# Kernel optimization log

Measured on AMD Instinct MI355X. Metric: run time of the kernel, lower is better.

## Reference

```python
import jax, jax.numpy as jnp
import numpy as np

L, D, H, N, R = 4, 256, 512, 16, 8  # layers, d_model, hidden=2*d_model, state_dim, dt_rank
OUT_LEN, IN_DIM = 96, 32
EPS = 1e-5


def _layernorm(v, g, b):
    m = jnp.mean(v, axis=-1, keepdims=True)
    var = jnp.mean((v - m) ** 2, axis=-1, keepdims=True)
    return (v - m) / jnp.sqrt(var + EPS) * g + b


def _pos_encoding(T, d):
    pos = jnp.arange(T, dtype=jnp.float32)[:, None]
    div = jnp.exp(jnp.arange(0, d, 2, dtype=jnp.float32) * (-np.log(10000.0) / d))
    pe = jnp.zeros((T, d), dtype=jnp.float32)
    pe = pe.at[:, 0::2].set(jnp.sin(pos * div))
    pe = pe.at[:, 1::2].set(jnp.cos(pos * div))
    return pe


def setup_inputs() -> dict:
    key = jax.random.key(0)
    ks = jax.random.split(key, 20)
    inp = {
        "x": jax.random.normal(ks[0], (8, 1024, IN_DIM), dtype=jnp.float32),
        "emb_w": jax.random.normal(ks[1], (D, IN_DIM), dtype=jnp.float32) * 0.1,
        "emb_b": jnp.zeros((D,), dtype=jnp.float32),
        "norm_g": jnp.ones((L, D), dtype=jnp.float32),
        "norm_b": jnp.zeros((L, D), dtype=jnp.float32),
        "in_w": jax.random.normal(ks[2], (L, H, D), dtype=jnp.float32) * (1.0 / np.sqrt(D)),
        "conv_w": jax.random.normal(ks[3], (L, H, 1, 3), dtype=jnp.float32) * 0.5,
        "A_p": jax.random.normal(ks[4], (L, H, N), dtype=jnp.float32) * 0.01,
        "D_p": jnp.ones((L, H), dtype=jnp.float32),
        "dt1_w": jax.random.normal(ks[5], (L, R, H), dtype=jnp.float32) * (1.0 / np.sqrt(H)),
        "dt1_b": jnp.zeros((L, R), dtype=jnp.float32),
        "dt2_w": jax.random.normal(ks[6], (L, H, R), dtype=jnp.float32) * (1.0 / np.sqrt(R)),
        "dt2_b": jnp.zeros((L, H), dtype=jnp.float32),
        "out_w": jax.random.normal(ks[7], (L, D, H), dtype=jnp.float32) * (1.0 / np.sqrt(H)),
        "final_g": jnp.ones((D,), dtype=jnp.float32),
        "final_b": jnp.zeros((D,), dtype=jnp.float32),
        "head1_w": jax.random.normal(ks[8], (D, D), dtype=jnp.float32) * (1.0 / np.sqrt(D)),
        "head1_b": jnp.zeros((D,), dtype=jnp.float32),
        "head2_w": jax.random.normal(ks[9], (OUT_LEN, D), dtype=jnp.float32) * (1.0 / np.sqrt(D)),
        "head2_b": jnp.zeros((OUT_LEN,), dtype=jnp.float32),
    }
    return inp


def _mamba_block(h, g, b, in_w, conv_w, A_p, D_p, dt1_w, dt1_b, dt2_w, dt2_b, out_w):
    res = h
    v = _layernorm(h, g, b)            # [B,T,D]
    v = jnp.einsum('btd,hd->bth', v, in_w)  # [B,T,H]
    # depthwise conv1d, kernel 3, padding 1, groups=H
    vc = jnp.transpose(v, (0, 2, 1))   # [B,H,T]
    vc = jax.lax.conv_general_dilated(vc, conv_w, window_strides=(1,),
                                      padding=[(1, 1)], feature_group_count=H,
                                      dimension_numbers=('NCH', 'OIH', 'NCH'))
    v = jnp.transpose(jax.nn.silu(vc), (0, 2, 1))  # [B,T,H]
    dt = jax.nn.relu(jnp.einsum('bth,rh->btr', v, dt1_w) + dt1_b)
    dt = jnp.einsum('btr,hr->bth', dt, dt2_w) + dt2_b
    dt = jax.nn.softplus(dt)           # [B,T,H]
    A = -jnp.exp(A_p)                  # [H,N]
    safe_A = jnp.where(jnp.abs(A) < 1e-5, jnp.ones_like(A), A)

    B_sz = v.shape[0]
    state0 = jnp.zeros((B_sz, H, N), dtype=v.dtype)

    def step(state, inp):
        x_t, dt_t = inp  # [B,H] each
        dA = A * dt_t[..., None]            # [B,H,N]
        discA = jnp.exp(dA)
        discB = (discA - 1.0) / safe_A * dt_t[..., None]
        state = discA * state + discB * x_t[..., None]
        y = jnp.einsum('bhn,hn->bh', state, A_p) + D_p * x_t
        return state, y

    xs = (jnp.transpose(v, (1, 0, 2)), jnp.transpose(dt, (1, 0, 2)))  # [T,B,H]
    _, ys = jax.lax.scan(step, state0, xs)
    y = jnp.transpose(ys, (1, 0, 2))   # [B,T,H]
    return res + jnp.einsum('bth,dh->btd', y, out_w)


def reference(x, emb_w, emb_b, norm_g, norm_b, in_w, conv_w, A_p, D_p,
              dt1_w, dt1_b, dt2_w, dt2_b, out_w, final_g, final_b,
              head1_w, head1_b, head2_w, head2_b):
    h = jnp.einsum('bti,di->btd', x, emb_w) + emb_b  # [B,T,D]
    h = h + _pos_encoding(h.shape[1], D)[None]
    for l in range(L):
        h = _mamba_block(h, norm_g[l], norm_b[l], in_w[l], conv_w[l], A_p[l],
                         D_p[l], dt1_w[l], dt1_b[l], dt2_w[l], dt2_b[l], out_w[l])
    h = _layernorm(h, final_g, final_b)
    h = h[:, -1, :]                    # last token [B,D]
    h = jax.nn.silu(h @ head1_w.T + head1_b)
    return h @ head2_w.T + head2_b     # [B, OUT_LEN]
```

## Files before the change

kernel.cpp:

```cpp
#include <hip/hip_runtime.h>
#include <hip/hip_bf16.h>
#include <math.h>

#define BB 8
#define TT 1024
#define DD 256
#define HH 512
#define NN 16
#define RR 8
#define OUT_LEN 96
#define IN_DIM 32
#define MM (BB*TT)

#define SC 16
#define CC (TT/SC)

typedef unsigned short u16;
typedef unsigned int u32;
typedef __attribute__((ext_vector_type(8))) short short8;
typedef __attribute__((ext_vector_type(8))) unsigned short u16x8;
typedef __attribute__((ext_vector_type(4))) float float4v;

__device__ __forceinline__ u16 f2bf(float f) {
    __hip_bfloat16 h = __float2bfloat16(f);
    return *(u16*)&h;
}
__device__ __forceinline__ float bf2f(u16 u) {
    u32 v = ((u32)u) << 16;
    return *(float*)&v;
}

#define GLD_LDS16(src, dst) __builtin_amdgcn_global_load_lds( \
    (const __attribute__((address_space(1))) void*)(src),     \
    (__attribute__((address_space(3))) void*)(dst), 16, 0, 0)

__global__ __launch_bounds__(256) void embed_ln_cvt_kernel(
    const float* __restrict__ x, const float* __restrict__ emb_w,
    const float* __restrict__ emb_b,
    const float* __restrict__ g, const float* __restrict__ b,
    float* __restrict__ h, u16* __restrict__ lnout,
    const float* __restrict__ w_in, u16* __restrict__ wbf_in,
    const float* __restrict__ w_out, u16* __restrict__ wbf_out, int nw)
{
    int bid = blockIdx.x;
    if (bid >= MM) {
        int i = (bid - MM) * 256 + threadIdx.x;
        if (i < nw) wbf_in[i] = f2bf(w_in[i]);
        else        wbf_out[i - nw] = f2bf(w_out[i - nw]);
        return;
    }

    int bt = bid;
    int d  = threadIdx.x;
    int t  = bt & (TT - 1);

    __shared__ float xs[IN_DIM];
    __shared__ float red[4], red2[4];
    if (threadIdx.x < IN_DIM) xs[threadIdx.x] = x[bt * IN_DIM + threadIdx.x];
    __syncthreads();

    const float* w = emb_w + d * IN_DIM;
    float acc = emb_b[d];
#pragma unroll
    for (int i = 0; i < IN_DIM; i++) acc = fmaf(xs[i], w[i], acc);

    int i2 = d & ~1;
    float div = __expf(-(float)i2 * 0.0359778918f);
    float arg = (float)t * div;
    float pe = (d & 1) ? __cosf(arg) : __sinf(arg);
    float val = acc + pe;
    h[bt * DD + d] = val;

    float s = val;
#pragma unroll
    for (int o = 32; o > 0; o >>= 1) s += __shfl_down(s, o);
    int lane = d & 63, wave = d >> 6;
    if (lane == 0) red[wave] = s;
    __syncthreads();
    float mean = (red[0] + red[1] + red[2] + red[3]) * (1.0f / DD);

    float c = val - mean;
    float s2 = c * c;
#pragma unroll
    for (int o = 32; o > 0; o >>= 1) s2 += __shfl_down(s2, o);
    if (lane == 0) red2[wave] = s2;
    __syncthreads();
    float var = (red2[0] + red2[1] + red2[2] + red2[3]) * (1.0f / DD);

    lnout[bt * DD + d] = f2bf(c * rsqrtf(var + 1e-5f) * g[d] + b[d]);
}

template<int BM, int BN, int OUT_BF16>
__global__ __launch_bounds__(256) void gemm_bf16(
    const u16* __restrict__ A, const u16* __restrict__ B,
    void* __restrict__ Cv, int M, int N, int K, int addC)
{
    constexpr int BK = 64;
    constexpr int MT = BM / 32;
    constexpr int NT = BN / 32;
    static_assert(BN == 64, "B staging assumes BN==64");

    __shared__ __align__(16) u16 Al[8][BM][8];
    __shared__ __align__(16) u16 Bl[8][BN][8];

    const int tid = threadIdx.x;
    const int nbx = gridDim.x;
    const int o   = blockIdx.x + nbx * blockIdx.y;
    const int r8  = o & 7, q8 = o >> 3;
    const int bxs = q8 % nbx;
    const int bys = (q8 / nbx) * 8 + r8;
    const int bm = bys * BM;
    const int bn = bxs * BN;
    const int wid = tid >> 6, lane = tid & 63;
    const int wm = wid >> 1, wn = wid & 1;
    const int lq = lane >> 4, lm = lane & 15;

    float4v acc[MT][NT];
#pragma unroll
    for (int i = 0; i < MT; i++)
#pragma unroll
        for (int j = 0; j < NT; j++) acc[i][j] = (float4v){0.f, 0.f, 0.f, 0.f};

    for (int k0 = 0; k0 < K; k0 += BK) {
#pragma unroll
        for (int it = 0; it < (8 * BM) / 256; it++) {
            int c = it * 256 + tid;
            int q = c / BM, row = c % BM;
            GLD_LDS16(A + (size_t)(bm + row) * K + k0 + q * 8, &Al[q][row][0]);
        }
#pragma unroll
        for (int it = 0; it < (8 * BN) / 256; it++) {
            int c = it * 256 + tid;
            int q = c / BN, row = c % BN;
            GLD_LDS16(B + (size_t)(bn + row) * K + k0 + q * 8, &Bl[q][row][0]);
        }
        __syncthreads();

        short8 af[2][MT], bf[2][NT];
#pragma unroll
        for (int kk = 0; kk < 2; kk++) {
#pragma unroll
            for (int mt = 0; mt < MT; mt++)
                af[kk][mt] = *(const short8*)&Al[kk * 4 + lq][wm * (BM / 2) + mt * 16 + lm][0];
#pragma unroll
            for (int nt = 0; nt < NT; nt++)
                bf[kk][nt] = *(const short8*)&Bl[kk * 4 + lq][wn * (BN / 2) + nt * 16 + lm][0];
        }

#pragma unroll
        for (int kk = 0; kk < 2; kk++)
#pragma unroll
            for (int mt = 0; mt < MT; mt++)
#pragma unroll
                for (int nt = 0; nt < NT; nt++)
                    acc[mt][nt] = __builtin_amdgcn_mfma_f32_16x16x32_bf16(
                        af[kk][mt], bf[kk][nt], acc[mt][nt], 0, 0, 0);
        __syncthreads();
    }

#pragma unroll
    for (int mt = 0; mt < MT; mt++)
#pragma unroll
        for (int nt = 0; nt < NT; nt++) {
            int row0 = bm + wm * (BM / 2) + mt * 16 + lq * 4;
            int col  = bn + wn * (BN / 2) + nt * 16 + lm;
#pragma unroll
            for (int r = 0; r < 4; r++) {
                float vv = acc[mt][nt][r];
                if (OUT_BF16) {
                    ((u16*)Cv)[(size_t)(row0 + r) * N + col] = f2bf(vv);
                } else {
                    float* cp = (float*)Cv + (size_t)(row0 + r) * N + col;
                    if (addC) vv += *cp;
                    *cp = vv;
                }
            }
        }
}

__global__ __launch_bounds__(256) void gemm2_ln(
    const u16* __restrict__ A, const u16* __restrict__ B,
    float* __restrict__ h,
    const float* __restrict__ g, const float* __restrict__ bb,
    u16* __restrict__ lnout, int doLN)
{
    constexpr int BM = 32;
    __shared__ __align__(16) u16 Al[8][BM][8];
    __shared__ __align__(16) u16 Bl[8][256][8];
    __shared__ float rs[2][BM], qs[2][BM];

    const int tid = threadIdx.x;
    const int bm = blockIdx.x * BM;
    const int wid = tid >> 6, lane = tid & 63;
    const int wm = wid >> 1, wn = wid & 1;
    const int lq = lane >> 4, lm = lane & 15;

    float4v acc[8];
#pragma unroll
    for (int j = 0; j < 8; j++) acc[j] = (float4v){0.f, 0.f, 0.f, 0.f};

    for (int k0 = 0; k0 < 512; k0 += 64) {
        {
            int q = tid >> 5, row = tid & 31;
            GLD_LDS16(A + (size_t)(bm + row) * 512 + k0 + q * 8, &Al[q][row][0]);
        }
#pragma unroll
        for (int it = 0; it < 8; it++) {
            int c = it * 256 + tid;
            int q = c >> 8, row = c & 255;
            GLD_LDS16(B + (size_t)row * 512 + k0 + q * 8, &Bl[q][row][0]);
        }
        __syncthreads();

        short8 af[2], bf[2][8];
#pragma unroll
        for (int kk = 0; kk < 2; kk++) {
            af[kk] = *(const short8*)&Al[kk * 4 + lq][wm * 16 + lm][0];
#pragma unroll
            for (int nt = 0; nt < 8; nt++)
                bf[kk][nt] = *(const short8*)&Bl[kk * 4 + lq][wn * 128 + nt * 16 + lm][0];
        }
#pragma unroll
        for (int kk = 0; kk < 2; kk++)
#pragma unroll
            for (int nt = 0; nt < 8; nt++)
                acc[nt] = __builtin_amdgcn_mfma_f32_16x16x32_bf16(
                    af[kk], bf[kk][nt], acc[nt], 0, 0, 0);
        __syncthreads();
    }

    float val[4][8];
    float s1[4] = {0.f, 0.f, 0.f, 0.f}, s2[4] = {0.f, 0.f, 0.f, 0.f};
#pragma unroll
    for (int r = 0; r < 4; r++) {
        int row = bm + wm * 16 + lq * 4 + r;
#pragma unroll
        for (int nt = 0; nt < 8; nt++) {
            int col = wn * 128 + nt * 16 + lm;
            float v = acc[nt][r] + h[(size_t)row * DD + col];
            val[r][nt] = v;
            s1[r] += v;
            s2[r] = fmaf(v, v, s2[r]);
            h[(size_t)row * DD + col] = v;
        }
    }
#pragma unroll
    for (int r = 0; r < 4; r++) {
#pragma unroll
        for (int o = 1; o < 16; o <<= 1) {
            s1[r] += __shfl_xor(s1[r], o);
            s2[r] += __shfl_xor(s2[r], o);
        }
    }
    if (lm == 0) {
#pragma unroll
        for (int r = 0; r < 4; r++) {
            rs[wn][wm * 16 + lq * 4 + r] = s1[r];
            qs[wn][wm * 16 + lq * 4 + r] = s2[r];
        }
    }
    __syncthreads();

    if (doLN) {
#pragma unroll
        for (int r = 0; r < 4; r++) {
            int i = wm * 16 + lq * 4 + r;
            int row = bm + i;
            float mean = (rs[0][i] + rs[1][i]) * (1.0f / DD);
            float var  = (qs[0][i] + qs[1][i]) * (1.0f / DD) - mean * mean;
            float rstd = rsqrtf(var + 1e-5f);
#pragma unroll
            for (int nt = 0; nt < 8; nt++) {
                int col = wn * 128 + nt * 16 + lm;
                lnout[(size_t)row * DD + col] =
                    f2bf((val[r][nt] - mean) * rstd * g[col] + bb[col]);
            }
        }
    }
}

__global__ __launch_bounds__(256) void conv_dt1_kernel(
    const u16* __restrict__ v, const float* __restrict__ cwg,
    const float* __restrict__ w1g, const float* __restrict__ b1g,
    u16* __restrict__ vsb, float* __restrict__ dtr)
{
    __shared__ float w1s[RR * 2 * 256];
    int tid = threadIdx.x;
    {
        int lane = tid & 63, rc = tid >> 6;
#pragma unroll
        for (int i = 0; i < 4; i++) {
            int rci = rc + i * 4;
            int r = rci >> 1, jc = rci & 1;
            float4 wv = *(const float4*)(w1g + r * HH + lane * 8 + jc * 4);
            *(float4*)&w1s[rci * 256 + lane * 4] = wv;
        }
    }
    __syncthreads();

    int wave = tid >> 6, lane = tid & 63;
    int m = blockIdx.x * 4 + wave;
    int t = m & (TT - 1);
    int h0 = lane * 8;

    const u16* vrow = v + (size_t)m * HH + h0;
    u16x8 x0 = *(const u16x8*)vrow;
    u16x8 xm = (t > 0)      ? *(const u16x8*)(vrow - HH) : (u16x8)(0);
    u16x8 xp = (t < TT - 1) ? *(const u16x8*)(vrow + HH) : (u16x8)(0);

    const float* wp = cwg + h0 * 3;
    float a[8];
    u16x8 o;
#pragma unroll
    for (int j = 0; j < 8; j++) {
        float s = wp[j * 3] * bf2f(xm[j]);
        s = fmaf(wp[j * 3 + 1], bf2f(x0[j]), s);
        s = fmaf(wp[j * 3 + 2], bf2f(xp[j]), s);
        s = s / (1.0f + __expf(-s));
        a[j] = s;
        o[j] = f2bf(s);
    }
    *(u16x8*)(vsb + (size_t)m * HH + h0) = o;

    float acc[RR];
#pragma unroll
    for (int r = 0; r < RR; r++) {
        float4 wlo = *(const float4*)&w1s[(r * 2 + 0) * 256 + lane * 4];
        float4 whi = *(const float4*)&w1s[(r * 2 + 1) * 256 + lane * 4];
        float s = a[0] * wlo.x;
        s = fmaf(a[1], wlo.y, s);
        s = fmaf(a[2], wlo.z, s);
        s = fmaf(a[3], wlo.w, s);
        s = fmaf(a[4], whi.x, s);
        s = fmaf(a[5], whi.y, s);
        s = fmaf(a[6], whi.z, s);
        s = fmaf(a[7], whi.w, s);
        acc[r] = s;
    }
#pragma unroll
    for (int r = 0; r < RR; r++) {
#pragma unroll
        for (int o2 = 1; o2 < 64; o2 <<= 1) acc[r] += __shfl_xor(acc[r], o2);
    }
    if (lane == 0) {
#pragma unroll
        for (int r = 0; r < RR; r++) acc[r] = fmaxf(acc[r] + b1g[r], 0.0f);
        *(float4*)(dtr + (size_t)m * RR)     = make_float4(acc[0], acc[1], acc[2], acc[3]);
        *(float4*)(dtr + (size_t)m * RR + 4) = make_float4(acc[4], acc[5], acc[6], acc[7]);
    }
}

__device__ __forceinline__ float softplus_f(float s) {
    return (s > 20.0f) ? s : __logf(1.0f + __expf(s));
}

__global__ __launch_bounds__(256, 4) void scan_pass1(
    const u16* __restrict__ vs, const float* __restrict__ dtr,
    const float* __restrict__ dt2_w, const float* __restrict__ dt2_b,
    const float* __restrict__ A_p,
    u16* __restrict__ Lst, float* __restrict__ sdt)
{
    int h = blockIdx.x * 256 + threadIdx.x;
    int c = blockIdx.y;
    int b = blockIdx.z;

    __shared__ float ds[SC * RR];
    {
        const float* drow = dtr + ((size_t)b * TT + (size_t)c * SC) * RR;
        if (threadIdx.x < SC * RR) ds[threadIdx.x] = drow[threadIdx.x];
    }

    float A2[NN], invA[NN], st[NN];
    const float* ap = A_p + h * NN;
#pragma unroll
    for (int n = 0; n < NN; n++) {
        float a = -__expf(ap[n]);
        A2[n] = a * 1.44269504f;
        invA[n] = 1.0f / a;
        st[n] = 0.0f;
    }
    float w2[RR];
#pragma unroll
    for (int r = 0; r < RR; r++) w2[r] = dt2_w[h * RR + r];
    float b2 = dt2_b[h];

    const u16* vbase = vs + ((size_t)b * TT + (size_t)c * SC) * HH + h;
    float xv = bf2f(vbase[0]);
    __syncthreads();

    float s_dt = 0.0f;
#pragma unroll 2
    for (int t = 0; t < SC; t++) {
        float xn = (t + 1 < SC) ? bf2f(vbase[(size_t)(t + 1) * HH]) : 0.0f;
        float s = b2;
#pragma unroll
        for (int r = 0; r < RR; r++) s = fmaf(ds[t * RR + r], w2[r], s);
        float dt = softplus_f(s);
        s_dt += dt;
        float dtx = dt * xv;
#pragma unroll
        for (int n = 0; n < NN; n++) {
            float e = __builtin_amdgcn_exp2f(A2[n] * dt);
            float u = invA[n] * dtx;
            st[n] = fmaf(e, st[n] + u, -u);
        }
        xv = xn;
    }

    size_t base = (((size_t)c * BB + b) * HH + h) * NN;
    u16x8 lo, hi;
#pragma unroll
    for (int n = 0; n < 8; n++) { lo[n] = f2bf(st[n]); hi[n] = f2bf(st[n + 8]); }
    *(u16x8*)(Lst + base)     = lo;
    *(u16x8*)(Lst + base + 8) = hi;
    sdt[((size_t)c * BB + b) * HH + h] = s_dt;
}

__global__ __launch_bounds__(256) void scan_carry_par(
    const float* __restrict__ A_p, const float* __restrict__ sdt,
    u16* __restrict__ Lst)
{
    int gw   = (blockIdx.x << 2) | (threadIdx.x >> 6);
    int lane = threadIdx.x & 63;
    int b = gw >> 9;
    int h = gw & 511;

    size_t sidx = ((size_t)lane * BB + b) * HH + h;
    float sd = sdt[sidx];
    const float* ap = A_p + h * NN;
    u16x8 Llo = *(const u16x8*)(Lst + sidx * NN);
    u16x8 Lhi = *(const u16x8*)(Lst + sidx * NN + 8);
    u16x8 Elo, Ehi;
#pragma unroll
    for (int n = 0; n < NN; n++) {
        float An = -__expf(ap[n]);
        float p  = __expf(An * sd);
        float lv = bf2f((n < 8) ? Llo[n] : Lhi[n - 8]);
#pragma unroll
        for (int d2 = 1; d2 < 64; d2 <<= 1) {
            float pp = __shfl_up(p, d2);
            float pl = __shfl_up(lv, d2);
            if (lane >= d2) { lv = fmaf(pl, p, lv); p = pp * p; }
        }
        float E = __shfl_up(lv, 1);
        if (lane == 0) E = 0.0f;
        if (n < 8) Elo[n] = f2bf(E); else Ehi[n - 8] = f2bf(E);
    }
    *(u16x8*)(Lst + sidx * NN)     = Elo;
    *(u16x8*)(Lst + sidx * NN + 8) = Ehi;
}

__global__ __launch_bounds__(256, 4) void scan_pass2(
    const u16* __restrict__ vs,
    const float* __restrict__ dtr,
    const float* __restrict__ dt2_w,
    const float* __restrict__ dt2_b,
    const float* __restrict__ A_p, const float* __restrict__ D_p,
    const u16* __restrict__ carry,
    u16* __restrict__ y)
{
    int h = blockIdx.x * 256 + threadIdx.x;
    int c = blockIdx.y;
    int b = blockIdx.z;

    __shared__ float ds[SC * RR];
    {
        const float* drow = dtr + ((size_t)b * TT + (size_t)c * SC) * RR;
        if (threadIdx.x < SC * RR) ds[threadIdx.x] = drow[threadIdx.x];
    }

    float A2[NN], invA[NN], Ap[NN], st[NN];
    const float* app = A_p + h * NN;
    size_t cbase = (((size_t)c * BB + b) * HH + h) * NN;
    {
        u16x8 lo = *(const u16x8*)(carry + cbase);
        u16x8 hi = *(const u16x8*)(carry + cbase + 8);
#pragma unroll
        for (int n = 0; n < 8; n++) { st[n] = bf2f(lo[n]); st[n + 8] = bf2f(hi[n]); }
    }
#pragma unroll
    for (int n = 0; n < NN; n++) {
        float apv = app[n];
        Ap[n] = apv;
        float a = -__expf(apv);
        A2[n] = a * 1.44269504f;
        invA[n] = 1.0f / a;
    }
    float w2[RR];
#pragma unroll
    for (int r = 0; r < RR; r++) w2[r] = dt2_w[h * RR + r];
    float b2 = dt2_b[h];
    float Dp = D_p[h];

    const u16* vbase = vs + ((size_t)b * TT + (size_t)c * SC) * HH + h;
    u16*       ybase = y  + ((size_t)b * TT + (size_t)c * SC) * HH + h;
    float xv = bf2f(vbase[0]);
    __syncthreads();

#pragma unroll 2
    for (int t = 0; t < SC; t++) {
        float xn = (t + 1 < SC) ? bf2f(vbase[(size_t)(t + 1) * HH]) : 0.0f;
        float s = b2;
#pragma unroll
        for (int r = 0; r < RR; r++) s = fmaf(ds[t * RR + r], w2[r], s);
        float dt = softplus_f(s);
        float dtx = dt * xv;
        float acc = Dp * xv;
#pragma unroll
        for (int n = 0; n < NN; n++) {
            float e = __builtin_amdgcn_exp2f(A2[n] * dt);
            float u = invA[n] * dtx;
            st[n] = fmaf(e, st[n] + u, -u);
            acc = fmaf(st[n], Ap[n], acc);
        }
        ybase[(size_t)t * HH] = f2bf(acc);
        xv = xn;
    }
}

__global__ __launch_bounds__(256) void head_kernel(
    const float* __restrict__ h,
    const float* __restrict__ fg, const float* __restrict__ fb,
    const float* __restrict__ w1, const float* __restrict__ b1,
    const float* __restrict__ w2, const float* __restrict__ b2,
    float* __restrict__ out)
{
    int b = blockIdx.x;
    int d = threadIdx.x;
    __shared__ float hn[DD], s1[DD];
    __shared__ float red[4];

    float v = h[((size_t)b * TT + (TT - 1)) * DD + d];

    float s = v;
#pragma unroll
    for (int o = 32; o > 0; o >>= 1) s += __shfl_down(s, o);
    int lane = d & 63, wave = d >> 6;
    if (lane == 0) red[wave] = s;
    __syncthreads();
    float mean = (red[0] + red[1] + red[2] + red[3]) * (1.0f / DD);
    __syncthreads();

    float c = v - mean;
    float s2 = c * c;
#pragma unroll
    for (int o = 32; o > 0; o >>= 1) s2 += __shfl_down(s2, o);
    if (lane == 0) red[wave] = s2;
    __syncthreads();
    float var = (red[0] + red[1] + red[2] + red[3]) * (1.0f / DD);

    hn[d] = c * rsqrtf(var + 1e-5f) * fg[d] + fb[d];
    __syncthreads();

    float a1 = b1[d];
    const float* w1r = w1 + d * DD;
#pragma unroll 8
    for (int k = 0; k < DD; k++) a1 = fmaf(hn[k], w1r[k], a1);
    s1[d] = a1 / (1.0f + __expf(-a1));
    __syncthreads();

    if (d < OUT_LEN) {
        float a2 = b2[d];
        const float* w2r = w2 + d * DD;
#pragma unroll 8
        for (int k = 0; k < DD; k++) a2 = fmaf(s1[k], w2r[k], a2);
        out[b * OUT_LEN + d] = a2;
    }
}

extern "C" void kernel_launch(void* const* d_in, const int* in_sizes, int n_in,
                              void* d_out, int out_size, void* d_ws, size_t ws_size,
                              hipStream_t stream)
{
    (void)in_sizes; (void)n_in; (void)out_size; (void)ws_size;

    const float* x       = (const float*)d_in[0];
    const float* emb_w   = (const float*)d_in[1];
    const float* emb_b   = (const float*)d_in[2];
    const float* norm_g  = (const float*)d_in[3];
    const float* norm_b  = (const float*)d_in[4];
    const float* in_w    = (const float*)d_in[5];
    const float* conv_w  = (const float*)d_in[6];
    const float* A_p     = (const float*)d_in[7];
    const float* D_p     = (const float*)d_in[8];
    const float* dt1_w   = (const float*)d_in[9];
    const float* dt1_b   = (const float*)d_in[10];
    const float* dt2_w   = (const float*)d_in[11];
    const float* dt2_b   = (const float*)d_in[12];
    const float* out_w   = (const float*)d_in[13];
    const float* final_g = (const float*)d_in[14];
    const float* final_b = (const float*)d_in[15];
    const float* head1_w = (const float*)d_in[16];
    const float* head1_b = (const float*)d_in[17];
    const float* head2_w = (const float*)d_in[18];
    const float* head2_b = (const float*)d_in[19];
    float* outp = (float*)d_out;

    char* ws = (char*)d_ws;
    float* h     = (float*)ws;                ws += (size_t)MM * DD * 4;
    u16*   vbf   = (u16*)ws;                  ws += (size_t)MM * HH * 2;
    u16*   vsb   = (u16*)ws;                  ws += (size_t)MM * HH * 2;
    u16*   ybf   = (u16*)ws;                  ws += (size_t)MM * HH * 2;
    u16*   lnbuf = (u16*)ws;                  ws += (size_t)MM * DD * 2;
    float* dtr   = (float*)ws;                ws += (size_t)MM * RR * 4;
    u16*   Lst   = (u16*)ws;                  ws += (size_t)CC * BB * HH * NN * 2;
    float* sdt   = (float*)ws;                ws += (size_t)CC * BB * HH * 4;
    u16*   wbf_in  = (u16*)ws;                ws += (size_t)4 * HH * DD * 2;
    u16*   wbf_out = (u16*)ws;                ws += (size_t)4 * DD * HH * 2;

    const int NW = 4 * HH * DD;
    embed_ln_cvt_kernel<<<MM + (2 * NW) / 256, 256, 0, stream>>>(
        x, emb_w, emb_b, norm_g, norm_b, h, lnbuf,
        in_w, wbf_in, out_w, wbf_out, NW);

    for (int l = 0; l < 4; l++) {
        gemm_bf16<128, 64, 1><<<dim3(HH / 64, MM / 128), 256, 0, stream>>>(
            lnbuf, wbf_in + (size_t)l * HH * DD, vbf, MM, HH, DD, 0);
        conv_dt1_kernel<<<MM / 4, 256, 0, stream>>>(
            vbf, conv_w + (size_t)l * HH * 3,
            dt1_w + (size_t)l * RR * HH, dt1_b + l * RR, vsb, dtr);

        scan_pass1<<<dim3(HH / 256, CC, BB), 256, 0, stream>>>(
            vsb, dtr, dt2_w + (size_t)l * HH * RR, dt2_b + l * HH,
            A_p + (size_t)l * HH * NN, Lst, sdt);
        scan_carry_par<<<(BB * HH) / 4, 256, 0, stream>>>(
            A_p + (size_t)l * HH * NN, sdt, Lst);
        scan_pass2<<<dim3(HH / 256, CC, BB), 256, 0, stream>>>(
            vsb, dtr, dt2_w + (size_t)l * HH * RR, dt2_b + l * HH,
            A_p + (size_t)l * HH * NN, D_p + l * HH, Lst, ybf);

        const float* g_next = (l < 3) ? (norm_g + (l + 1) * DD) : final_g;
        const float* b_next = (l < 3) ? (norm_b + (l + 1) * DD) : final_b;
        gemm2_ln<<<MM / 32, 256, 0, stream>>>(
            ybf, wbf_out + (size_t)l * DD * HH, h, g_next, b_next,
            lnbuf, (l < 3) ? 1 : 0);
    }

    head_kernel<<<BB, 256, 0, stream>>>(h, final_g, final_b,
                                        head1_w, head1_b, head2_w, head2_b, outp);
}
```

Measured before the change: 499.4 us.

## Double-buffer LDS tiles in bf16 GEMMs to prefetch next K slice

Both the generic bf16 GEMM and the fused GEMM+LayerNorm kernel now keep two LDS buffers for the A and B tiles. They load the first K slice before the loop, then issue loads for the next slice before running the MFMAs on the current one, so global-to-LDS traffic can overlap with matrix math and one barrier per iteration is dropped. The generic GEMM also drops its grouped block-index swizzle in favour of plain blockIdx mapping, which may reduce L2 reuse. The doubled LDS footprint, about 64KB for B in gemm2_ln, can lower occupancy.

```diff
diff --git a/kernel.cpp b/kernel.cpp
--- a/kernel.cpp
+++ b/kernel.cpp
@@ -100,17 +100,12 @@
     constexpr int NT = BN / 32;
     static_assert(BN == 64, "B staging assumes BN==64");
 
-    __shared__ __align__(16) u16 Al[8][BM][8];
-    __shared__ __align__(16) u16 Bl[8][BN][8];
+    __shared__ __align__(16) u16 Al[2][8][BM][8];
+    __shared__ __align__(16) u16 Bl[2][8][BN][8];
 
     const int tid = threadIdx.x;
-    const int nbx = gridDim.x;
-    const int o   = blockIdx.x + nbx * blockIdx.y;
-    const int r8  = o & 7, q8 = o >> 3;
-    const int bxs = q8 % nbx;
-    const int bys = (q8 / nbx) * 8 + r8;
-    const int bm = bys * BM;
-    const int bn = bxs * BN;
+    const int bm = blockIdx.y * BM;
+    const int bn = blockIdx.x * BN;
     const int wid = tid >> 6, lane = tid & 63;
     const int wm = wid >> 1, wn = wid & 1;
     const int lq = lane >> 4, lm = lane & 15;
@@ -121,30 +116,47 @@
 #pragma unroll
         for (int j = 0; j < NT; j++) acc[i][j] = (float4v){0.f, 0.f, 0.f, 0.f};
 
+#pragma unroll
+    for (int it = 0; it < (8 * BM) / 256; it++) {
+        int c = it * 256 + tid;
+        int q = c / BM, row = c % BM;
+        GLD_LDS16(A + (size_t)(bm + row) * K + q * 8, &Al[0][q][row][0]);
+    }
+#pragma unroll
+    for (int it = 0; it < (8 * BN) / 256; it++) {
+        int c = it * 256 + tid;
+        int q = c / BN, row = c % BN;
+        GLD_LDS16(B + (size_t)(bn + row) * K + q * 8, &Bl[0][q][row][0]);
+    }
+    __syncthreads();
+
+    int cur = 0;
     for (int k0 = 0; k0 < K; k0 += BK) {
-#pragma unroll
-        for (int it = 0; it < (8 * BM) / 256; it++) {
-            int c = it * 256 + tid;
-            int q = c / BM, row = c % BM;
-            GLD_LDS16(A + (size_t)(bm + row) * K + k0 + q * 8, &Al[q][row][0]);
-        }
-#pragma unroll
-        for (int it = 0; it < (8 * BN) / 256; it++) {
-            int c = it * 256 + tid;
-            int q = c / BN, row = c % BN;
-            GLD_LDS16(B + (size_t)(bn + row) * K + k0 + q * 8, &Bl[q][row][0]);
-        }
-        __syncthreads();
+        if (k0 + BK < K) {
+            int nxt = cur ^ 1;
+#pragma unroll
+            for (int it = 0; it < (8 * BM) / 256; it++) {
+                int c = it * 256 + tid;
+                int q = c / BM, row = c % BM;
+                GLD_LDS16(A + (size_t)(bm + row) * K + k0 + BK + q * 8, &Al[nxt][q][row][0]);
+            }
+#pragma unroll
+            for (int it = 0; it < (8 * BN) / 256; it++) {
+                int c = it * 256 + tid;
+                int q = c / BN, row = c % BN;
+                GLD_LDS16(B + (size_t)(bn + row) * K + k0 + BK + q * 8, &Bl[nxt][q][row][0]);
+            }
+        }
 
         short8 af[2][MT], bf[2][NT];
 #pragma unroll
         for (int kk = 0; kk < 2; kk++) {
 #pragma unroll
             for (int mt = 0; mt < MT; mt++)
-                af[kk][mt] = *(const short8*)&Al[kk * 4 + lq][wm * (BM / 2) + mt * 16 + lm][0];
+                af[kk][mt] = *(const short8*)&Al[cur][kk * 4 + lq][wm * (BM / 2) + mt * 16 + lm][0];
 #pragma unroll
             for (int nt = 0; nt < NT; nt++)
-                bf[kk][nt] = *(const short8*)&Bl[kk * 4 + lq][wn * (BN / 2) + nt * 16 + lm][0];
+                bf[kk][nt] = *(const short8*)&Bl[cur][kk * 4 + lq][wn * (BN / 2) + nt * 16 + lm][0];
         }
 
 #pragma unroll
@@ -156,6 +168,7 @@
                     acc[mt][nt] = __builtin_amdgcn_mfma_f32_16x16x32_bf16(
                         af[kk][mt], bf[kk][nt], acc[mt][nt], 0, 0, 0);
         __syncthreads();
+        cur ^= 1;
     }
 
 #pragma unroll
@@ -185,8 +198,8 @@
     u16* __restrict__ lnout, int doLN)
 {
     constexpr int BM = 32;
-    __shared__ __align__(16) u16 Al[8][BM][8];
-    __shared__ __align__(16) u16 Bl[8][256][8];
+    __shared__ __align__(16) u16 Al[2][8][BM][8];
+    __shared__ __align__(16) u16 Bl[2][8][256][8];
     __shared__ float rs[2][BM], qs[2][BM];
 
     const int tid = threadIdx.x;
@@ -199,26 +212,41 @@
 #pragma unroll
     for (int j = 0; j < 8; j++) acc[j] = (float4v){0.f, 0.f, 0.f, 0.f};
 
+    {
+        int q = tid >> 5, row = tid & 31;
+        GLD_LDS16(A + (size_t)(bm + row) * 512 + q * 8, &Al[0][q][row][0]);
+    }
+#pragma unroll
+    for (int it = 0; it < 8; it++) {
+        int c = it * 256 + tid;
+        int q = c >> 8, row = c & 255;
+        GLD_LDS16(B + (size_t)row * 512 + q * 8, &Bl[0][q][row][0]);
+    }
+    __syncthreads();
+
+    int cur = 0;
     for (int k0 = 0; k0 < 512; k0 += 64) {
-        {
-            int q = tid >> 5, row = tid & 31;
-            GLD_LDS16(A + (size_t)(bm + row) * 512 + k0 + q * 8, &Al[q][row][0]);
-        }
-#pragma unroll
-        for (int it = 0; it < 8; it++) {
-            int c = it * 256 + tid;
-            int q = c >> 8, row = c & 255;
-            GLD_LDS16(B + (size_t)row * 512 + k0 + q * 8, &Bl[q][row][0]);
-        }
-        __syncthreads();
+        if (k0 + 64 < 512) {
+            int nxt = cur ^ 1;
+            {
+                int q = tid >> 5, row = tid & 31;
+                GLD_LDS16(A + (size_t)(bm + row) * 512 + k0 + 64 + q * 8, &Al[nxt][q][row][0]);
+            }
+#pragma unroll
+            for (int it = 0; it < 8; it++) {
+                int c = it * 256 + tid;
+                int q = c >> 8, row = c & 255;
+                GLD_LDS16(B + (size_t)row * 512 + k0 + 64 + q * 8, &Bl[nxt][q][row][0]);
+            }
+        }
 
         short8 af[2], bf[2][8];
 #pragma unroll
         for (int kk = 0; kk < 2; kk++) {
-            af[kk] = *(const short8*)&Al[kk * 4 + lq][wm * 16 + lm][0];
+            af[kk] = *(const short8*)&Al[cur][kk * 4 + lq][wm * 16 + lm][0];
 #pragma unroll
             for (int nt = 0; nt < 8; nt++)
-                bf[kk][nt] = *(const short8*)&Bl[kk * 4 + lq][wn * 128 + nt * 16 + lm][0];
+                bf[kk][nt] = *(const short8*)&Bl[cur][kk * 4 + lq][wn * 128 + nt * 16 + lm][0];
         }
 #pragma unroll
         for (int kk = 0; kk < 2; kk++)
@@ -227,6 +255,7 @@
                 acc[nt] = __builtin_amdgcn_mfma_f32_16x16x32_bf16(
                     af[kk], bf[kk][nt], acc[nt], 0, 0, 0);
         __syncthreads();
+        cur ^= 1;
     }
 
     float val[4][8];
```

Measured after the change: 498.8 us. Within noise of the previous version (-0.1%).
